# Optimization experiments

Measured on AMD Instinct MI355X. Metric: run time of the kernel, lower is better.

The kernel has to match this reference:

```python
import jax, jax.numpy as jnp
import numpy as np

B, T, D_IN = 1024, 128, 256
H = 128          # hidden_dim == memory_unit_size (required by einsum)
M = 128          # memory_units == memory_unit_size (required by view)
W = 128          # memory_unit_size
R = 4            # read_heads
OUT = 2


def setup_inputs() -> dict:
    key = jax.random.key(0)
    ks = jax.random.split(key, 9)
    s = 0.05
    return {
        "x": jax.random.normal(ks[0], (B, T, D_IN), dtype=jnp.float32),
        "memory": jax.random.normal(ks[1], (M, W), dtype=jnp.float32) * s,
        "read_vectors0": jax.random.normal(ks[2], (R, W), dtype=jnp.float32) * s,
        "W_ih": jax.random.normal(ks[3], (4 * H, D_IN + R * W), dtype=jnp.float32) * s,
        "W_hh": jax.random.normal(ks[4], (4 * H, H), dtype=jnp.float32) * s,
        "b_ih": jax.random.normal(ks[5], (4 * H,), dtype=jnp.float32) * s,
        "b_hh": jax.random.normal(ks[6], (4 * H,), dtype=jnp.float32) * s,
        "fc_w": jax.random.normal(ks[7], (OUT, H + R * W), dtype=jnp.float32) * s,
        "fc_b": jax.random.normal(ks[8], (OUT,), dtype=jnp.float32) * s,
    }


def reference(x, memory, read_vectors0, W_ih, W_hh, b_ih, b_hh, fc_w, fc_b):
    batch = x.shape[0]
    # softmax over memory slots (dim=0), constant across timesteps
    mem_sm = jax.nn.softmax(memory, axis=0)  # [M, W]
    bias = b_ih + b_hh

    # initial read vectors: [R, W] -> repeat over batch -> flatten [B, R*W]
    rv = jnp.tile(read_vectors0[None], (batch, 1, 1)).reshape(batch, R * W)
    h0 = jnp.zeros((batch, H), x.dtype)
    c0 = jnp.zeros((batch, H), x.dtype)

    def step(carry, xt):
        h, c, rv = carry
        inp = jnp.concatenate([xt, rv], axis=-1)           # [B, D_IN+R*W]
        gates = inp @ W_ih.T + h @ W_hh.T + bias           # [B, 4H]
        i, f, g, o = jnp.split(gates, 4, axis=-1)          # torch LSTM gate order
        c = jax.nn.sigmoid(f) * c + jax.nn.sigmoid(i) * jnp.tanh(g)
        h = jax.nn.sigmoid(o) * jnp.tanh(c)                # [B, H]
        read = jnp.einsum('ij,kj->ki', mem_sm, h)          # [B, M]
        # faithful to torch: repeat to [R, B, M] then view(B, R*M) (mixes rows)
        rv_new = jnp.broadcast_to(read[None], (R, batch, M)).reshape(batch, R * M)
        out = jnp.concatenate([h, rv_new], axis=-1) @ fc_w.T + fc_b  # [B, OUT]
        return (h, c, rv_new), out

    _, outs = jax.lax.scan(step, (h0, c0, rv), jnp.swapaxes(x, 0, 1))  # [T, B, OUT]
    return outs.mean(axis=0)  # [B, OUT]
```

## Files before the change

kernel.cpp:

```cpp
#include <hip/hip_runtime.h>

#define BB 1024
#define TT 128
#define NBLK 256

using bf16   = __bf16;
using bf16x8 = __attribute__((ext_vector_type(8))) bf16;
using bf16x4 = __attribute__((ext_vector_type(4))) bf16;
using f32x4  = __attribute__((ext_vector_type(4))) float;

__device__ __forceinline__ float fsig(float x) {
  return __builtin_amdgcn_rcpf(1.f + __expf(-x));
}
__device__ __forceinline__ float ftanh(float x) {
  return 2.f * __builtin_amdgcn_rcpf(1.f + __expf(-2.f * x)) - 1.f;
}

__device__ __forceinline__ void st_u32_coh(unsigned* p, unsigned v) {
  __hip_atomic_store(p, v, __ATOMIC_RELAXED, __HIP_MEMORY_SCOPE_AGENT);
}
__device__ __forceinline__ unsigned ld_u32_coh(const unsigned* p) {
  return __hip_atomic_load((unsigned*)p, __ATOMIC_RELAXED, __HIP_MEMORY_SCOPE_AGENT);
}
__device__ __forceinline__ float ld_f32_coh(const float* p) {
  return __hip_atomic_load((float*)p, __ATOMIC_RELAXED, __HIP_MEMORY_SCOPE_AGENT);
}
__device__ __forceinline__ void st_f32_coh(float* p, float v) {
  __hip_atomic_store(p, v, __ATOMIC_RELAXED, __HIP_MEMORY_SCOPE_AGENT);
}
__device__ __forceinline__ void st_u16_coh(unsigned short* p, unsigned short v) {
  __hip_atomic_store(p, v, __ATOMIC_RELAXED, __HIP_MEMORY_SCOPE_AGENT);
}
__device__ __forceinline__ bf16x8 ld_bf16x8_coh(const bf16* p) {
  union { unsigned long long u[2]; bf16x8 v; } c;
  c.u[0] = __hip_atomic_load((unsigned long long*)p, __ATOMIC_RELAXED, __HIP_MEMORY_SCOPE_AGENT);
  c.u[1] = __hip_atomic_load((unsigned long long*)(p + 4), __ATOMIC_RELAXED, __HIP_MEMORY_SCOPE_AGENT);
  return c.v;
}

__global__ void prep_a(const float* __restrict__ x, const float* __restrict__ mem,
                       const float* __restrict__ b_ih, const float* __restrict__ b_hh,
                       const float* __restrict__ rv0, const float* __restrict__ W_ih,
                       bf16* __restrict__ x_bf, float* __restrict__ mem_sm,
                       float* __restrict__ bias, float* __restrict__ G0,
                       unsigned* __restrict__ slots) {
  const int bid = blockIdx.x, tid = threadIdx.x;
  if (bid < 2048) {
    const int lane = tid & 63, wv = tid >> 6;
    const int wg = bid * 4 + wv;
#pragma unroll 4
    for (int r = 0; r < 16; ++r) {
      int rid = wg + r * 8192;
      int b = rid >> 7, t = rid & 127;
      int rowp = ((b >> 4) & 15) * 64 + (b >> 8) * 16 + (b & 15);
      const float4 v = *(const float4*)(x + (size_t)rid * 256 + lane * 4);
      bf16x4 o;
      o[0] = (bf16)v.x; o[1] = (bf16)v.y; o[2] = (bf16)v.z; o[3] = (bf16)v.w;
      *(bf16x4*)(x_bf + ((size_t)t * BB + rowp) * 256 + lane * 4) = o;
    }
  } else if (bid == 2048) {
    __shared__ float sM[128 * 128];
    for (int e = tid; e < 16384; e += 256) sM[e] = mem[e];
    __syncthreads();
    if (tid < 128) {
      float mx = -1e30f;
      for (int m = 0; m < 128; ++m) mx = fmaxf(mx, sM[m * 128 + tid]);
      float s = 0.f;
      for (int m = 0; m < 128; ++m) s += __expf(sM[m * 128 + tid] - mx);
      float inv = 1.f / s;
      for (int m = 0; m < 128; ++m) mem_sm[m * 128 + tid] = __expf(sM[m * 128 + tid] - mx) * inv;
    }
  } else if (bid == 2049) {
    for (int e = tid; e < 512; e += 256) bias[e] = b_ih[e] + b_hh[e];
  } else if (bid < 2052) {
    int g = (bid - 2050) * 256 + tid;
    float acc = 0.f;
    for (int k = 0; k < 512; ++k) acc += rv0[k] * W_ih[(size_t)g * 768 + 256 + k];
    G0[g] = acc;
  } else {
    for (int e = tid; e < 4096; e += 256) slots[e] = 0u;
  }
}

__global__ void prep_b(const float* __restrict__ W_ih, const float* __restrict__ fc_w,
                       const float* __restrict__ mem_sm,
                       bf16* __restrict__ WMg, float* __restrict__ FM) {
  const int bid = blockIdx.x, tid = threadIdx.x;
  if (bid < 512) {
    __shared__ float sW[512];
    const int g = bid;
    for (int e = tid; e < 512; e += 256) sW[e] = W_ih[(size_t)g * 768 + 256 + e];
    __syncthreads();
    const int r = tid >> 6, n0 = (tid & 63) * 2;
    float a0 = 0.f, a1 = 0.f;
    const float* wr = sW + r * 128;
#pragma unroll 4
    for (int m = 0; m < 128; ++m) {
      float2 ms = *(const float2*)(mem_sm + m * 128 + n0);
      a0 += wr[m] * ms.x;
      a1 += wr[m] * ms.y;
    }
    union { bf16 h[2]; unsigned u; } pk;
    pk.h[0] = (bf16)a0; pk.h[1] = (bf16)a1;
    *(unsigned*)(WMg + (size_t)g * 512 + r * 128 + n0) = pk.u;
  } else {
    for (int sub = tid; sub < 2 * 512; sub += 256) {
      int o = sub >> 9, rn = sub & 511, rr = rn >> 7, n = rn & 127;
      const float* wr = fc_w + o * 640 + 128 + rr * 128;
      float acc = 0.f;
      for (int m = 0; m < 128; ++m) acc += wr[m] * mem_sm[m * 128 + n];
      FM[o * 512 + rn] = acc;
    }
  }
}

__global__ void __launch_bounds__(256, 1) dnc_main(
    const bf16* __restrict__ x_bf, const bf16* __restrict__ WMg,
    const float* __restrict__ bias, const float* __restrict__ G0,
    const float* __restrict__ FM, bf16* __restrict__ hbuf0, bf16* __restrict__ hbuf1,
    float* __restrict__ hsumG, unsigned* __restrict__ slots,
    const float* __restrict__ W_ih, const float* __restrict__ W_hh,
    const float* __restrict__ fc_w, const float* __restrict__ fc_b,
    float* __restrict__ out) {
  __shared__ bf16 sWx[32][264];
  __shared__ bf16 sWhh[32][136];
  __shared__ bf16 sWM[32][520];
  __shared__ bf16 sHq[16][520];

  const int bid = blockIdx.x, tid = threadIdx.x;
  const int rt = bid >> 4, gt = bid & 15;
  const int wave = tid >> 6, lane = tid & 63;
  const int l15 = lane & 15, l4 = lane >> 4;

  auto gcol = [&](int pos) { return ((pos >> 3) << 7) + gt * 8 + (pos & 7); };

  for (int e = tid; e < 32 * 256; e += 256) sWx[e >> 8][e & 255] = (bf16)W_ih[(size_t)gcol(e >> 8) * 768 + (e & 255)];
  for (int e = tid; e < 32 * 128; e += 256) sWhh[e >> 7][e & 127] = (bf16)W_hh[gcol(e >> 7) * 128 + (e & 127)];
  for (int e = tid; e < 32 * 512; e += 256) sWM[e >> 9][e & 511] = WMg[(size_t)gcol(e >> 9) * 512 + (e & 511)];
  __syncthreads();

  const float bv0 = bias[gcol(l15)], bv1 = bias[gcol(16 + l15)];

  const bool lo = (l15 < 8);
  const int j = l15 & 7;
  const int rb = lo ? 0 : 2;
  float cst[2] = {0.f, 0.f}, hsum[2] = {0.f, 0.f};
  int growp[2];
#pragma unroll
  for (int k = 0; k < 2; ++k) growp[k] = rt * 16 + (l4 * 4 + rb + k) + 256 * wave;

  f32x4 acc0, acc1;

  auto xpart = [&](int t) {
    acc0 = f32x4{bv0, bv0, bv0, bv0};
    acc1 = f32x4{bv1, bv1, bv1, bv1};
    const bf16* xr = x_bf + ((size_t)t * BB + rt * 64 + wave * 16 + l15) * 256 + l4 * 8;
#pragma unroll
    for (int kk = 0; kk < 8; ++kk) {
      bf16x8 a  = *(const bf16x8*)(xr + kk * 32);
      bf16x8 w0 = *(const bf16x8*)&sWx[l15][kk * 32 + l4 * 8];
      bf16x8 w1 = *(const bf16x8*)&sWx[16 + l15][kk * 32 + l4 * 8];
      acc0 = __builtin_amdgcn_mfma_f32_16x16x32_bf16(a, w0, acc0, 0, 0, 0);
      acc1 = __builtin_amdgcn_mfma_f32_16x16x32_bf16(a, w1, acc1, 0, 0, 0);
    }
  };

  auto hpart = [&](const bf16* hrd) {
    bf16x8 ha[4];
    const bf16* hr = hrd + (size_t)(rt * 16 + l15 + 256 * wave) * 128 + l4 * 8;
#pragma unroll
    for (int kk = 0; kk < 4; ++kk) ha[kk] = ld_bf16x8_coh(hr + kk * 32);
#pragma unroll
    for (int pass = 0; pass < 4; ++pass) {
      int row = (tid >> 4) + 16 * pass, seg = tid & 15;
      bf16x8 v = ld_bf16x8_coh(hrd + (size_t)(rt * 64 + row) * 128 + seg * 8);
      *(bf16x8*)&sHq[row >> 2][(row & 3) * 128 + seg * 8] = v;
    }
#pragma unroll
    for (int kk = 0; kk < 4; ++kk) {
      bf16x8 w0 = *(const bf16x8*)&sWhh[l15][kk * 32 + l4 * 8];
      bf16x8 w1 = *(const bf16x8*)&sWhh[16 + l15][kk * 32 + l4 * 8];
      acc0 = __builtin_amdgcn_mfma_f32_16x16x32_bf16(ha[kk], w0, acc0, 0, 0, 0);
      acc1 = __builtin_amdgcn_mfma_f32_16x16x32_bf16(ha[kk], w1, acc1, 0, 0, 0);
    }
    __syncthreads();
#pragma unroll
    for (int kk = 0; kk < 16; ++kk) {
      bf16x8 a  = *(const bf16x8*)&sHq[l15][kk * 32 + l4 * 8];
      bf16x8 w0 = *(const bf16x8*)&sWM[l15][kk * 32 + l4 * 8];
      bf16x8 w1 = *(const bf16x8*)&sWM[16 + l15][kk * 32 + l4 * 8];
      acc0 = __builtin_amdgcn_mfma_f32_16x16x32_bf16(a, w0, acc0, 0, 0, 0);
      acc1 = __builtin_amdgcn_mfma_f32_16x16x32_bf16(a, w1, acc1, 0, 0, 0);
    }
  };

  auto pw = [&](bool add_g0, bf16* hwr) {
    float o0[4], o1[4];
#pragma unroll
    for (int r = 0; r < 4; ++r) {
      o0[r] = __shfl_xor(acc0[r], 8);
      o1[r] = __shfl_xor(acc1[r], 8);
    }
    float g0i = 0.f, g0f = 0.f, g0g = 0.f, g0o = 0.f;
    if (add_g0) {
      int cb = gt * 8 + j;
      g0i = G0[cb]; g0f = G0[128 + cb]; g0g = G0[256 + cb]; g0o = G0[384 + cb];
    }
#pragma unroll
    for (int k = 0; k < 2; ++k) {
      int r = rb + k;
      float gi = (lo ? acc0[r] : o0[r]) + g0i;
      float gf = (lo ? o0[r] : acc0[r]) + g0f;
      float gg = (lo ? acc1[r] : o1[r]) + g0g;
      float go = (lo ? o1[r] : acc1[r]) + g0o;
      cst[k] = fsig(gf) * cst[k] + fsig(gi) * ftanh(gg);
      float h = fsig(go) * ftanh(cst[k]);
      hsum[k] += h;
      union { bf16 b; unsigned short u; } cv; cv.b = (bf16)h;
      st_u16_coh((unsigned short*)(hwr + (size_t)growp[k] * 128 + gt * 8 + j), cv.u);
    }
  };

  auto commit = [&](unsigned gen) {
    asm volatile("s_waitcnt vmcnt(0)" ::: "memory");
    __syncthreads();
    if (tid == 0) st_u32_coh(slots + bid * 16, gen);
  };
  auto gridwait = [&](unsigned gen) {
    while (ld_u32_coh(slots + tid * 16) < gen) {}
    __syncthreads();
  };

  xpart(0);
  pw(true, hbuf0);
  commit(1);
  for (int t = 1; t < TT; ++t) {
    xpart(t);
    gridwait(t);
    hpart((t & 1) ? hbuf0 : hbuf1);
    pw(false, (t & 1) ? hbuf1 : hbuf0);
    commit(t + 1);
  }
#pragma unroll
  for (int k = 0; k < 2; ++k)
    st_f32_coh(hsumG + (size_t)growp[k] * 128 + gt * 8 + j, hsum[k]);
  commit(TT + 1);
  gridwait(TT + 1);
  {
    int row = bid * 4 + wave;
    const float* hsr = hsumG + (size_t)row * 128;
    const float* hqr = hsumG + (size_t)(row & 255) * 512;
    float s0 = 0.f, s1 = 0.f;
    for (int k = lane; k < 128; k += 64) { float v = ld_f32_coh(hsr + k); s0 += v * fc_w[k]; s1 += v * fc_w[640 + k]; }
    for (int k = lane; k < 512; k += 64) { float v = ld_f32_coh(hqr + k); s0 += v * FM[k]; s1 += v * FM[512 + k]; }
    for (int off = 32; off > 0; off >>= 1) { s0 += __shfl_down(s0, off); s1 += __shfl_down(s1, off); }
    if (lane == 0) {
      out[row * 2 + 0] = s0 * (1.f / 128.f) + fc_b[0];
      out[row * 2 + 1] = s1 * (1.f / 128.f) + fc_b[1];
    }
  }
}

extern "C" void kernel_launch(void* const* d_in, const int* in_sizes, int n_in,
                              void* d_out, int out_size, void* d_ws, size_t ws_size,
                              hipStream_t stream) {
  const float* x      = (const float*)d_in[0];
  const float* memory = (const float*)d_in[1];
  const float* rv0    = (const float*)d_in[2];
  const float* W_ih   = (const float*)d_in[3];
  const float* W_hh   = (const float*)d_in[4];
  const float* b_ih   = (const float*)d_in[5];
  const float* b_hh   = (const float*)d_in[6];
  const float* fc_w   = (const float*)d_in[7];
  const float* fc_b   = (const float*)d_in[8];
  float* out = (float*)d_out;
  char* ws = (char*)d_ws;

  bf16*     x_bf   = (bf16*)ws;
  bf16*     WMg    = (bf16*)(ws + 67108864);
  float*    mem_sm = (float*)(ws + 67633152);
  float*    bias   = (float*)(ws + 67698688);
  float*    G0     = (float*)(ws + 67700736);
  float*    FM     = (float*)(ws + 67702784);
  bf16*     hbuf0  = (bf16*)(ws + 67706880);
  bf16*     hbuf1  = (bf16*)(ws + 67969024);
  unsigned* slots  = (unsigned*)(ws + 68231168);
  float*    hsumG  = (float*)(ws + 68247552);

  prep_a<<<2053, 256, 0, stream>>>(x, memory, b_ih, b_hh, rv0, W_ih,
                                   x_bf, mem_sm, bias, G0, slots);
  prep_b<<<513, 256, 0, stream>>>(W_ih, fc_w, mem_sm, WMg, FM);
  dnc_main<<<NBLK, 256, 0, stream>>>(x_bf, WMg, bias, G0, FM, hbuf0, hbuf1, hsumG, slots,
                                     W_ih, W_hh, fc_w, fc_b, out);
}
```

Measured before the change: 842.9 us.

## Fold weight preprocessing into main kernel and poll grid barrier with one wave

Removes the prep_b kernel and the small prep_a branches. Each main block now computes the memory softmax, the W_ih·softmax product (via MFMA into shared memory), the fc·softmax projection and the initial-read gate term itself, and sums the biases inline. The grid barrier poll is changed so that a single wave checks all 256 slots with four loads per lane, instead of every thread spinning on one slot. This saves a kernel launch and global round-trips, but every block redundantly recomputes the softmax and projections, which lengthens the prologue.

```diff
diff --git a/kernel.cpp b/kernel.cpp
--- a/kernel.cpp
+++ b/kernel.cpp
@@ -16,11 +16,11 @@
   return 2.f * __builtin_amdgcn_rcpf(1.f + __expf(-2.f * x)) - 1.f;
 }
 
-__device__ __forceinline__ void st_u32_coh(unsigned* p, unsigned v) {
+__device__ __forceinline__ void st_i32_coh(int* p, int v) {
   __hip_atomic_store(p, v, __ATOMIC_RELAXED, __HIP_MEMORY_SCOPE_AGENT);
 }
-__device__ __forceinline__ unsigned ld_u32_coh(const unsigned* p) {
-  return __hip_atomic_load((unsigned*)p, __ATOMIC_RELAXED, __HIP_MEMORY_SCOPE_AGENT);
+__device__ __forceinline__ int ld_i32_coh(const int* p) {
+  return __hip_atomic_load((int*)p, __ATOMIC_RELAXED, __HIP_MEMORY_SCOPE_AGENT);
 }
 __device__ __forceinline__ float ld_f32_coh(const float* p) {
   return __hip_atomic_load((float*)p, __ATOMIC_RELAXED, __HIP_MEMORY_SCOPE_AGENT);
@@ -38,94 +38,42 @@
   return c.v;
 }
 
-__global__ void prep_a(const float* __restrict__ x, const float* __restrict__ mem,
-                       const float* __restrict__ b_ih, const float* __restrict__ b_hh,
-                       const float* __restrict__ rv0, const float* __restrict__ W_ih,
-                       bf16* __restrict__ x_bf, float* __restrict__ mem_sm,
-                       float* __restrict__ bias, float* __restrict__ G0,
-                       unsigned* __restrict__ slots) {
-  const int bid = blockIdx.x, tid = threadIdx.x;
-  if (bid < 2048) {
-    const int lane = tid & 63, wv = tid >> 6;
-    const int wg = bid * 4 + wv;
+__global__ void x_convert(const float* __restrict__ x, bf16* __restrict__ x_bf,
+                          int* __restrict__ slots) {
+  const int tid = threadIdx.x, bid = blockIdx.x;
+  if (bid == 0) {
+    for (int e = tid; e < 4096; e += 256) st_i32_coh(slots + e, 0);
+  }
+  const int lane = tid & 63, wv = tid >> 6;
+  const int wg = bid * 4 + wv;
 #pragma unroll 4
-    for (int r = 0; r < 16; ++r) {
-      int rid = wg + r * 8192;
-      int b = rid >> 7, t = rid & 127;
-      int rowp = ((b >> 4) & 15) * 64 + (b >> 8) * 16 + (b & 15);
-      const float4 v = *(const float4*)(x + (size_t)rid * 256 + lane * 4);
-      bf16x4 o;
-      o[0] = (bf16)v.x; o[1] = (bf16)v.y; o[2] = (bf16)v.z; o[3] = (bf16)v.w;
-      *(bf16x4*)(x_bf + ((size_t)t * BB + rowp) * 256 + lane * 4) = o;
-    }
-  } else if (bid == 2048) {
-    __shared__ float sM[128 * 128];
-    for (int e = tid; e < 16384; e += 256) sM[e] = mem[e];
-    __syncthreads();
-    if (tid < 128) {
-      float mx = -1e30f;
-      for (int m = 0; m < 128; ++m) mx = fmaxf(mx, sM[m * 128 + tid]);
-      float s = 0.f;
-      for (int m = 0; m < 128; ++m) s += __expf(sM[m * 128 + tid] - mx);
-      float inv = 1.f / s;
-      for (int m = 0; m < 128; ++m) mem_sm[m * 128 + tid] = __expf(sM[m * 128 + tid] - mx) * inv;
-    }
-  } else if (bid == 2049) {
-    for (int e = tid; e < 512; e += 256) bias[e] = b_ih[e] + b_hh[e];
-  } else if (bid < 2052) {
-    int g = (bid - 2050) * 256 + tid;
-    float acc = 0.f;
-    for (int k = 0; k < 512; ++k) acc += rv0[k] * W_ih[(size_t)g * 768 + 256 + k];
-    G0[g] = acc;
-  } else {
-    for (int e = tid; e < 4096; e += 256) slots[e] = 0u;
-  }
-}
-
-__global__ void prep_b(const float* __restrict__ W_ih, const float* __restrict__ fc_w,
-                       const float* __restrict__ mem_sm,
-                       bf16* __restrict__ WMg, float* __restrict__ FM) {
-  const int bid = blockIdx.x, tid = threadIdx.x;
-  if (bid < 512) {
-    __shared__ float sW[512];
-    const int g = bid;
-    for (int e = tid; e < 512; e += 256) sW[e] = W_ih[(size_t)g * 768 + 256 + e];
-    __syncthreads();
-    const int r = tid >> 6, n0 = (tid & 63) * 2;
-    float a0 = 0.f, a1 = 0.f;
-    const float* wr = sW + r * 128;
-#pragma unroll 4
-    for (int m = 0; m < 128; ++m) {
-      float2 ms = *(const float2*)(mem_sm + m * 128 + n0);
-      a0 += wr[m] * ms.x;
-      a1 += wr[m] * ms.y;
-    }
-    union { bf16 h[2]; unsigned u; } pk;
-    pk.h[0] = (bf16)a0; pk.h[1] = (bf16)a1;
-    *(unsigned*)(WMg + (size_t)g * 512 + r * 128 + n0) = pk.u;
-  } else {
-    for (int sub = tid; sub < 2 * 512; sub += 256) {
-      int o = sub >> 9, rn = sub & 511, rr = rn >> 7, n = rn & 127;
-      const float* wr = fc_w + o * 640 + 128 + rr * 128;
-      float acc = 0.f;
-      for (int m = 0; m < 128; ++m) acc += wr[m] * mem_sm[m * 128 + n];
-      FM[o * 512 + rn] = acc;
-    }
+  for (int r = 0; r < 16; ++r) {
+    int rid = wg + r * 8192;
+    int b = rid >> 7, t = rid & 127;
+    int rowp = ((b >> 4) & 15) * 64 + (b >> 8) * 16 + (b & 15);
+    const float4 v = *(const float4*)(x + (size_t)rid * 256 + lane * 4);
+    bf16x4 o;
+    o[0] = (bf16)v.x; o[1] = (bf16)v.y; o[2] = (bf16)v.z; o[3] = (bf16)v.w;
+    *(bf16x4*)(x_bf + ((size_t)t * BB + rowp) * 256 + lane * 4) = o;
   }
 }
 
 __global__ void __launch_bounds__(256, 1) dnc_main(
-    const bf16* __restrict__ x_bf, const bf16* __restrict__ WMg,
-    const float* __restrict__ bias, const float* __restrict__ G0,
-    const float* __restrict__ FM, bf16* __restrict__ hbuf0, bf16* __restrict__ hbuf1,
-    float* __restrict__ hsumG, unsigned* __restrict__ slots,
+    const bf16* __restrict__ x_bf, const float* __restrict__ memf,
+    const float* __restrict__ rv0,
     const float* __restrict__ W_ih, const float* __restrict__ W_hh,
+    const float* __restrict__ b_ih, const float* __restrict__ b_hh,
     const float* __restrict__ fc_w, const float* __restrict__ fc_b,
+    bf16* __restrict__ hbuf0, bf16* __restrict__ hbuf1,
+    float* __restrict__ hsumG, int* __restrict__ slots,
     float* __restrict__ out) {
   __shared__ bf16 sWx[32][264];
   __shared__ bf16 sWhh[32][136];
   __shared__ bf16 sWM[32][520];
   __shared__ bf16 sHq[16][520];
+  __shared__ bf16 smT[128][136];
+  __shared__ float sFM[2][512];
+  __shared__ float sG0[32];
 
   const int bid = blockIdx.x, tid = threadIdx.x;
   const int rt = bid >> 4, gt = bid & 15;
@@ -136,10 +84,76 @@
 
   for (int e = tid; e < 32 * 256; e += 256) sWx[e >> 8][e & 255] = (bf16)W_ih[(size_t)gcol(e >> 8) * 768 + (e & 255)];
   for (int e = tid; e < 32 * 128; e += 256) sWhh[e >> 7][e & 127] = (bf16)W_hh[gcol(e >> 7) * 128 + (e & 127)];
-  for (int e = tid; e < 32 * 512; e += 256) sWM[e >> 9][e & 511] = WMg[(size_t)gcol(e >> 9) * 512 + (e & 511)];
+  if (tid < 128) {
+    const int n = tid;
+    float mx = -1e30f;
+    for (int m = 0; m < 128; ++m) mx = fmaxf(mx, memf[m * 128 + n]);
+    float s = 0.f;
+    for (int m = 0; m < 128; ++m) s += __expf(memf[m * 128 + n] - mx);
+    float inv = __builtin_amdgcn_rcpf(s);
+    float fa[8] = {0.f, 0.f, 0.f, 0.f, 0.f, 0.f, 0.f, 0.f};
+#pragma unroll 4
+    for (int m = 0; m < 128; ++m) {
+      float e = __expf(memf[m * 128 + n] - mx) * inv;
+      smT[n][m] = (bf16)e;
+#pragma unroll
+      for (int o = 0; o < 2; ++o)
+#pragma unroll
+        for (int r = 0; r < 4; ++r) fa[o * 4 + r] += e * fc_w[o * 640 + 128 + r * 128 + m];
+    }
+#pragma unroll
+    for (int o = 0; o < 2; ++o)
+#pragma unroll
+      for (int r = 0; r < 4; ++r) sFM[o][r * 128 + n] = fa[o * 4 + r];
+  }
+  if (tid < 32) {
+    const int c = tid >> 3, jj = tid & 7;
+    const float* wr = W_ih + (size_t)(c * 128 + gt * 8 + jj) * 768 + 256;
+    float acc = 0.f;
+#pragma unroll 4
+    for (int k4 = 0; k4 < 128; ++k4) {
+      float4 a = *(const float4*)(rv0 + k4 * 4);
+      float4 b = *(const float4*)(wr + k4 * 4);
+      acc += a.x * b.x + a.y * b.y + a.z * b.z + a.w * b.w;
+    }
+    sG0[tid] = acc;
+  }
   __syncthreads();
-
-  const float bv0 = bias[gcol(l15)], bv1 = bias[gcol(16 + l15)];
+#pragma unroll
+  for (int r = 0; r < 4; ++r) {
+    bf16x8 afr[2][4];
+#pragma unroll
+    for (int g = 0; g < 2; ++g)
+#pragma unroll
+      for (int kk = 0; kk < 4; ++kk) {
+        const float* ap = W_ih + (size_t)gcol(g * 16 + l15) * 768 + 256 + r * 128 + kk * 32 + l4 * 8;
+        float4 p0 = *(const float4*)ap, p1 = *(const float4*)(ap + 4);
+        bf16x8 f;
+        f[0] = (bf16)p0.x; f[1] = (bf16)p0.y; f[2] = (bf16)p0.z; f[3] = (bf16)p0.w;
+        f[4] = (bf16)p1.x; f[5] = (bf16)p1.y; f[6] = (bf16)p1.z; f[7] = (bf16)p1.w;
+        afr[g][kk] = f;
+      }
+#pragma unroll
+    for (int nto = 0; nto < 2; ++nto) {
+      const int nt = wave * 2 + nto;
+      f32x4 a0 = {0.f, 0.f, 0.f, 0.f}, a1 = {0.f, 0.f, 0.f, 0.f};
+#pragma unroll
+      for (int kk = 0; kk < 4; ++kk) {
+        bf16x8 b = *(const bf16x8*)&smT[nt * 16 + l15][kk * 32 + l4 * 8];
+        a0 = __builtin_amdgcn_mfma_f32_16x16x32_bf16(afr[0][kk], b, a0, 0, 0, 0);
+        a1 = __builtin_amdgcn_mfma_f32_16x16x32_bf16(afr[1][kk], b, a1, 0, 0, 0);
+      }
+#pragma unroll
+      for (int reg = 0; reg < 4; ++reg) {
+        sWM[l4 * 4 + reg][r * 128 + nt * 16 + l15]      = (bf16)a0[reg];
+        sWM[16 + l4 * 4 + reg][r * 128 + nt * 16 + l15] = (bf16)a1[reg];
+      }
+    }
+  }
+  __syncthreads();
+
+  const float bv0 = b_ih[gcol(l15)] + b_hh[gcol(l15)];
+  const float bv1 = b_ih[gcol(16 + l15)] + b_hh[gcol(16 + l15)];
 
   const bool lo = (l15 < 8);
   const int j = l15 & 7;
@@ -203,8 +217,7 @@
     }
     float g0i = 0.f, g0f = 0.f, g0g = 0.f, g0o = 0.f;
     if (add_g0) {
-      int cb = gt * 8 + j;
-      g0i = G0[cb]; g0f = G0[128 + cb]; g0g = G0[256 + cb]; g0o = G0[384 + cb];
+      g0i = sG0[j]; g0f = sG0[8 + j]; g0g = sG0[16 + j]; g0o = sG0[24 + j];
     }
 #pragma unroll
     for (int k = 0; k < 2; ++k) {
@@ -221,13 +234,21 @@
     }
   };
 
-  auto commit = [&](unsigned gen) {
+  auto commit = [&](int gen) {
     asm volatile("s_waitcnt vmcnt(0)" ::: "memory");
     __syncthreads();
-    if (tid == 0) st_u32_coh(slots + bid * 16, gen);
-  };
-  auto gridwait = [&](unsigned gen) {
-    while (ld_u32_coh(slots + tid * 16) < gen) {}
+    if (tid == 0) st_i32_coh(slots + bid * 16, gen);
+  };
+  auto gridwait = [&](int gen) {
+    if (wave == 0) {
+      int s0, s1, s2, s3;
+      do {
+        s0 = ld_i32_coh(slots + lane * 16);
+        s1 = ld_i32_coh(slots + (lane + 64) * 16);
+        s2 = ld_i32_coh(slots + (lane + 128) * 16);
+        s3 = ld_i32_coh(slots + (lane + 192) * 16);
+      } while (min(min(s0, s1), min(s2, s3)) < gen);
+    }
     __syncthreads();
   };
 
@@ -252,7 +273,7 @@
     const float* hqr = hsumG + (size_t)(row & 255) * 512;
     float s0 = 0.f, s1 = 0.f;
     for (int k = lane; k < 128; k += 64) { float v = ld_f32_coh(hsr + k); s0 += v * fc_w[k]; s1 += v * fc_w[640 + k]; }
-    for (int k = lane; k < 512; k += 64) { float v = ld_f32_coh(hqr + k); s0 += v * FM[k]; s1 += v * FM[512 + k]; }
+    for (int k = lane; k < 512; k += 64) { float v = ld_f32_coh(hqr + k); s0 += v * sFM[0][k]; s1 += v * sFM[1][k]; }
     for (int off = 32; off > 0; off >>= 1) { s0 += __shfl_down(s0, off); s1 += __shfl_down(s1, off); }
     if (lane == 0) {
       out[row * 2 + 0] = s0 * (1.f / 128.f) + fc_b[0];
@@ -276,20 +297,13 @@
   float* out = (float*)d_out;
   char* ws = (char*)d_ws;
 
-  bf16*     x_bf   = (bf16*)ws;
-  bf16*     WMg    = (bf16*)(ws + 67108864);
-  float*    mem_sm = (float*)(ws + 67633152);
-  float*    bias   = (float*)(ws + 67698688);
-  float*    G0     = (float*)(ws + 67700736);
-  float*    FM     = (float*)(ws + 67702784);
-  bf16*     hbuf0  = (bf16*)(ws + 67706880);
-  bf16*     hbuf1  = (bf16*)(ws + 67969024);
-  unsigned* slots  = (unsigned*)(ws + 68231168);
-  float*    hsumG  = (float*)(ws + 68247552);
-
-  prep_a<<<2053, 256, 0, stream>>>(x, memory, b_ih, b_hh, rv0, W_ih,
-                                   x_bf, mem_sm, bias, G0, slots);
-  prep_b<<<513, 256, 0, stream>>>(W_ih, fc_w, mem_sm, WMg, FM);
-  dnc_main<<<NBLK, 256, 0, stream>>>(x_bf, WMg, bias, G0, FM, hbuf0, hbuf1, hsumG, slots,
-                                     W_ih, W_hh, fc_w, fc_b, out);
-}
+  bf16* x_bf   = (bf16*)ws;
+  bf16* hbuf0  = (bf16*)(ws + 67108864);
+  bf16* hbuf1  = (bf16*)(ws + 67371008);
+  int*  slots  = (int*)(ws + 67633152);
+  float* hsumG = (float*)(ws + 67649536);
+
+  x_convert<<<2048, 256, 0, stream>>>(x, x_bf, slots);
+  dnc_main<<<NBLK, 256, 0, stream>>>(x_bf, memory, rv0, W_ih, W_hh, b_ih, b_hh,
+                                     fc_w, fc_b, hbuf0, hbuf1, hsumG, slots, out);
+}
```

Result: slower. 925.3 us (+9.8%).
